# Kernel tuning notes

Measured on AMD Instinct MI355X. Metric: run time of the kernel, lower is better.

## Reference

```python
import jax, jax.numpy as jnp
import numpy as np

ACT_BITS = 8
Q_B = 2 ** (ACT_BITS - 1)          # 128
EPS = 1e-6                          # module epsilon
GN_EPS = 1e-5                       # torch GroupNorm default eps
SCALE = 0.01                        # fixed ternary weight scale (buffer)
STRIDE = 1
PADDING = 1


def setup_inputs() -> dict:
    key = jax.random.key(0)
    k1, k2 = jax.random.split(key)
    x = jax.random.normal(k1, (16, 256, 64, 64), dtype=jnp.float32)
    weight = jax.random.normal(k2, (256, 256, 3, 3), dtype=jnp.float32)
    bias = jnp.zeros((256,), dtype=jnp.float32)
    ln_weight = jnp.ones((256,), dtype=jnp.float32)
    ln_bias = jnp.zeros((256,), dtype=jnp.float32)
    return {"x": x, "weight": weight, "bias": bias,
            "ln_weight": ln_weight, "ln_bias": ln_bias}


def _group_norm_1group(x, gamma, beta):
    # GroupNorm(1, C): normalize over (C, H, W) per sample, per-channel affine.
    mean = jnp.mean(x, axis=(1, 2, 3), keepdims=True)
    var = jnp.var(x, axis=(1, 2, 3), keepdims=True)
    xn = (x - mean) * jax.lax.rsqrt(var + GN_EPS)
    return xn * gamma[None, :, None, None] + beta[None, :, None, None]


def reference(x, weight, bias, ln_weight, ln_bias):
    # 1) GroupNorm
    x_ln = _group_norm_1group(x, ln_weight, ln_bias)

    # 2) BitNet absmax activation quantization (global absmax)
    gamma = jnp.maximum(jnp.max(jnp.abs(x_ln)), EPS)
    x_scaled = x_ln * (Q_B / gamma)
    x_clipped = jnp.clip(x_scaled, -Q_B + EPS, Q_B - EPS)
    x_quant = jnp.round(x_clipped)

    # 3) Ternary weight quantization with fixed scale: {-SCALE, 0, +SCALE}
    delta = 0.7 * jnp.mean(jnp.abs(weight))  # TTQ threshold
    w_q = jnp.where(weight > delta, SCALE,
                    jnp.where(weight < -delta, -SCALE, 0.0)).astype(weight.dtype)

    # 4) Conv2d (NCHW, OIHW)
    y = jax.lax.conv_general_dilated(
        x_quant, w_q,
        window_strides=(STRIDE, STRIDE),
        padding=[(PADDING, PADDING), (PADDING, PADDING)],
        dimension_numbers=("NCHW", "OIHW", "NCHW"),
        feature_group_count=1,
    )

    # 5) Dequant + bias
    y = y * (gamma / Q_B) + bias[None, :, None, None]
    return y
```

## Files before the change

kernel.cpp:

```cpp
#include <hip/hip_runtime.h>
#include <hip/hip_bf16.h>

#define CHW   1048576
#define XQ_BYTES 17842176u
#define WQ_OFF   17842176u
#define GNP_OFF  18432000u
#define CMM_OFF  18448384u
#define MR_OFF   18481152u
#define SC_OFF   18481280u
#define WP_OFF   18481296u
#define DL_OFF   18481584u
#define EVC_OFF  18481588u
#define EVL_OFF  18481592u

typedef __attribute__((ext_vector_type(4)))  int i32x4;
typedef __attribute__((ext_vector_type(16))) int i32x16;

__device__ __forceinline__ void gload16(const void* g, void* l) {
    __builtin_amdgcn_global_load_lds(
        (const __attribute__((address_space(1))) unsigned int*)(unsigned long long)(g),
        (__attribute__((address_space(3))) unsigned int*)(unsigned int)(unsigned long long)(l),
        16, 0, 0);
}

__global__ void k_pass1(const float* __restrict__ x, double2* __restrict__ part,
                        float2* __restrict__ cmm) {
    int bid = blockIdx.x;
    int n = bid >> 6, c4 = bid & 63;
    int t = threadIdx.x, ch = t >> 6, lane = t & 63;
    int c = c4 * 4 + ch;
    const float4* p = (const float4*)(x + (size_t)n * CHW + (size_t)c * 4096);
    double s = 0.0, ss = 0.0;
    float mn = 1e30f, mx = -1e30f;
#pragma unroll
    for (int k = 0; k < 16; ++k) {
        float4 v = p[k * 64 + lane];
        mn = fminf(mn, fminf(fminf(v.x, v.y), fminf(v.z, v.w)));
        mx = fmaxf(mx, fmaxf(fmaxf(v.x, v.y), fmaxf(v.z, v.w)));
        double dx = v.x, dy = v.y, dz = v.z, dw = v.w;
        s  += dx + dy + dz + dw;
        ss += dx * dx + dy * dy + dz * dz + dw * dw;
    }
    for (int o = 32; o; o >>= 1) {
        s += __shfl_down(s, o); ss += __shfl_down(ss, o);
        mn = fminf(mn, __shfl_down(mn, o)); mx = fmaxf(mx, __shfl_down(mx, o));
    }
    __shared__ double sh0[4], sh1[4];
    if (lane == 0) {
        cmm[n * 256 + c] = make_float2(mn, mx);
        sh0[ch] = s; sh1[ch] = ss;
    }
    __syncthreads();
    if (t == 0)
        part[bid] = make_double2(sh0[0] + sh0[1] + sh0[2] + sh0[3],
                                 sh1[0] + sh1[1] + sh1[2] + sh1[3]);
}

__global__ void k_wsum(const float* __restrict__ w, double* __restrict__ wp) {
    int blk = blockIdx.x, t = threadIdx.x;
    const float4* p = (const float4*)(w + (size_t)blk * 16384);
    double s = 0.0;
#pragma unroll
    for (int j = 0; j < 16; ++j) {
        float4 v = p[j * 256 + t];
        s += fabs((double)v.x) + fabs((double)v.y) + fabs((double)v.z) + fabs((double)v.w);
    }
    for (int o = 32; o; o >>= 1) s += __shfl_down(s, o);
    __shared__ double sh[4];
    if ((t & 63) == 0) sh[t >> 6] = s;
    __syncthreads();
    if (t == 0) wp[blk] = sh[0] + sh[1] + sh[2] + sh[3];
}

__global__ void k_scalars(const double2* __restrict__ part, const float2* __restrict__ cmm,
                          const float* __restrict__ lnw, const float* __restrict__ lnb,
                          const double* __restrict__ wp,
                          float2* __restrict__ mr, float* __restrict__ sc,
                          float* __restrict__ dl, int* __restrict__ evcnt) {
    __shared__ float shm[16], shr[16];
    int t = threadIdx.x;
    {
        int n = t >> 4, i = t & 15;
        double s = 0.0, ss = 0.0;
#pragma unroll
        for (int k = 0; k < 4; ++k) {
            double2 v = part[n * 64 + i * 4 + k];
            s += v.x; ss += v.y;
        }
        for (int o = 8; o; o >>= 1) { s += __shfl_down(s, o); ss += __shfl_down(ss, o); }
        if (i == 0) {
            double mean = s * (1.0 / 1048576.0);
            double var  = ss * (1.0 / 1048576.0) - mean * mean;
            shm[n] = (float)mean; shr[n] = (float)(1.0 / sqrt(var + 1e-5));
        }
    }
    __syncthreads();
    if (t < 16) mr[t] = make_float2(shm[t], shr[t]);
    if (t == 0) evcnt[0] = 0;
    float m = 0.0f;
#pragma unroll
    for (int k = 0; k < 16; ++k) {
        int idx = t + k * 256;
        int n = idx >> 8, c = idx & 255;
        float2 v = cmm[idx];
        float scale = lnw[c] * shr[n];
        float shift = lnb[c] - shm[n] * scale;
        m = fmaxf(m, fmaxf(fabsf(v.x * scale + shift), fabsf(v.y * scale + shift)));
    }
    for (int o = 32; o; o >>= 1) m = fmaxf(m, __shfl_down(m, o));
    __shared__ float shg[4];
    if ((t & 63) == 0) shg[t >> 6] = m;
    __syncthreads();
    if (t == 0) {
        float gamma = fmaxf(fmaxf(fmaxf(shg[0], shg[1]), fmaxf(shg[2], shg[3])), 1e-6f);
        sc[0] = gamma;
        sc[1] = 128.0f / gamma;
        sc[2] = (gamma / 128.0f) * 0.01f;
    }
    if (t < 64) {
        double s = (t < 36) ? wp[t] : 0.0;
        for (int o = 32; o; o >>= 1) s += __shfl_down(s, o);
        if (t == 0) dl[0] = (float)(0.7 * (s / 589824.0));
    }
}

__global__ void k_wquant(const float* __restrict__ w, const float* __restrict__ dl,
                         signed char* __restrict__ wq) {
    __shared__ float sw[2304];
    int co = blockIdx.x, t = threadIdx.x;
    const float* wr = w + (size_t)co * 2304;
#pragma unroll
    for (int j = 0; j < 9; ++j) sw[j * 256 + t] = wr[j * 256 + t];
    __syncthreads();
    float d = dl[0];
#pragma unroll
    for (int tap = 0; tap < 9; ++tap) {
        float v = sw[t * 9 + tap];
        int s = (v > d) ? 1 : ((v < -d) ? -1 : 0);
        wq[tap * 65536 + co * 256 + t] = (signed char)s;
    }
}

__global__ void k_halo(unsigned char* __restrict__ xq) {
    int idx = blockIdx.x * 8 + (threadIdx.x >> 5);
    int n = idx / 260, p = idx - n * 260;
    int hh, ww;
    if (p < 66)       { hh = 0;        ww = p; }
    else if (p < 132) { hh = 65;       ww = p - 66; }
    else if (p < 196) { hh = p - 131;  ww = 0; }
    else              { hh = p - 195;  ww = 65; }
    *(uint2*)(xq + ((size_t)(n * 66 + hh) * 66 + ww) * 256 + (threadIdx.x & 31) * 8) =
        make_uint2(0, 0);
}

__global__ void k_quantx(const float* __restrict__ x, const float2* __restrict__ mr,
                         const float* __restrict__ sc, const float* __restrict__ lnw,
                         const float* __restrict__ lnb, unsigned char* __restrict__ xq,
                         int* __restrict__ evcnt, int* __restrict__ evlist) {
    int bid = blockIdx.x;
    int n = bid >> 6, hg = (bid >> 2) & 15, cg = bid & 3;
    int t = threadIdx.x;
    int w = t & 63, h = hg * 4 + (t >> 6);
    float2 m = mr[n];
    float s128 = sc[1];
    uint u[16];
    const float* xp = x + (((size_t)n * 256 + cg * 64) * 64 + h) * 64 + w;
#pragma unroll
    for (int ci = 0; ci < 64; ++ci) {
        int c = cg * 64 + ci;
        float g = lnw[c] * m.y;
        float be = lnb[c];
        float v = xp[(size_t)ci * 4096];
        float xs = ((v - m.x) * g + be) * s128;
        xs = fminf(fmaxf(xs, -(128.0f - 1e-6f)), 128.0f - 1e-6f);
        int q = (int)rintf(xs);
        if (q == 128) {
            int idx = atomicAdd(evcnt, 1);
            if (idx < 1024) evlist[idx] = (n << 20) | (h << 14) | (w << 8) | c;
            q = 127;
        }
        uint b = (uint)(q & 255);
        if ((ci & 3) == 0) u[ci >> 2] = b; else u[ci >> 2] |= b << ((ci & 3) * 8);
    }
    unsigned char* op = xq + ((size_t)(n * 66 + h + 1) * 66 + (w + 1)) * 256 + cg * 64;
    uint4* o4 = (uint4*)op;
#pragma unroll
    for (int s2 = 0; s2 < 4; ++s2)
        o4[s2] = make_uint4(u[s2 * 4], u[s2 * 4 + 1], u[s2 * 4 + 2], u[s2 * 4 + 3]);
}

__global__ void k_fix(const signed char* __restrict__ wq, const int* __restrict__ evcnt,
                      const int* __restrict__ evlist, const float* __restrict__ sc,
                      float* __restrict__ out) {
    int cnt = *evcnt; if (cnt > 1024) cnt = 1024;
    float qs = sc[2];
    int co = threadIdx.x;
    for (int e = blockIdx.x; e < cnt; e += gridDim.x) {
        int pk = evlist[e];
        int n = pk >> 20, h = (pk >> 14) & 63, w = (pk >> 8) & 63, ci = pk & 255;
#pragma unroll
        for (int ty = 0; ty < 3; ++ty)
#pragma unroll
            for (int tx = 0; tx < 3; ++tx) {
                int i = h + 1 - ty, j = w + 1 - tx;
                if (i < 0 || i > 63 || j < 0 || j > 63) continue;
                int sgn = wq[(ty * 3 + tx) * 65536 + co * 256 + ci];
                if (sgn)
                    atomicAdd(out + (((size_t)n * 256 + co) * 64 + i) * 64 + j,
                              qs * (float)sgn);
            }
    }
}

#define ABUFB 32768
#define LD16(off) (*(const i32x4*)&lds8[(off)])
#define MFMA_I8(A, B, C) __builtin_amdgcn_mfma_i32_32x32x32_i8(A, B, C, 0, 0, 0)

#define STAGE_A(AS) { \
    const int _so = (AS) * ABUFB + wv * 1024; \
    gload16(aSrc + stA,         lds8 + _so); \
    gload16(aSrc + stA + 33792, lds8 + _so + 8192); \
    if (aKc < 3) { aKc++; stA += 64; } \
    else { aKc = 0; if (aTx < 2) { aTx++; stA += 64; } else { aTx = 0; stA += 16192; } } }

#define STAGE_B(BS) { \
    const int _so = (BS) * ABUFB + 16384 + wv * 1024; \
    gload16(bSrc + stB,         lds8 + _so); \
    gload16(bSrc + stB + 32768, lds8 + _so + 8192); \
    if (bKc < 3) { bKc++; stB += 64; } else { bKc = 0; stB += 65344; } }

#define STEP(R) { \
    const int _ab = (R) * ABUFB; \
    const int _bb = (R) * ABUFB + 16384; \
    i32x4 b00 = LD16(_bb + rdB);          i32x4 b01 = LD16((_bb + rdB) ^ 32); \
    i32x4 b10 = LD16(_bb + rdB + 2048);   i32x4 b11 = LD16((_bb + rdB + 2048) ^ 32); \
    _Pragma("unroll") \
    for (int _m = 0; _m < 4; ++_m) { \
        const int _ra = _ab + rdA + _m * 2048; \
        i32x4 a0 = LD16(_ra); \
        i32x4 a1 = LD16(_ra ^ 32); \
        __builtin_amdgcn_s_setprio(1); \
        acc[_m][0] = MFMA_I8(a0, b00, acc[_m][0]); \
        acc[_m][1] = MFMA_I8(a0, b10, acc[_m][1]); \
        acc[_m][0] = MFMA_I8(a1, b01, acc[_m][0]); \
        acc[_m][1] = MFMA_I8(a1, b11, acc[_m][1]); \
        __builtin_amdgcn_s_setprio(0); \
    } }

#define PITER(R0, R1, S0, S1, DO0, DO1, W) { \
    if (DO0) { STAGE_A(S0) STAGE_B(S0) } \
    if (DO1) { STAGE_A(S1) STAGE_B(S1) } \
    STEP(R0) \
    STEP(R1) \
    if ((W) == 4)      { asm volatile("s_waitcnt vmcnt(4)" ::: "memory"); } \
    else if ((W) == 0) { asm volatile("s_waitcnt vmcnt(0)" ::: "memory"); } \
    if ((W) >= 0) { __builtin_amdgcn_s_barrier(); __builtin_amdgcn_sched_barrier(0); } \
}

#define STORE4(P, A, BV) { \
    float4 v0; v0.x = (float)(A)[0]*qs+(BV);  v0.y = (float)(A)[1]*qs+(BV);  v0.z = (float)(A)[2]*qs+(BV);  v0.w = (float)(A)[3]*qs+(BV);  *(float4*)((P))      = v0; \
    float4 v1; v1.x = (float)(A)[4]*qs+(BV);  v1.y = (float)(A)[5]*qs+(BV);  v1.z = (float)(A)[6]*qs+(BV);  v1.w = (float)(A)[7]*qs+(BV);  *(float4*)((P) + 8)  = v1; \
    float4 v2; v2.x = (float)(A)[8]*qs+(BV);  v2.y = (float)(A)[9]*qs+(BV);  v2.z = (float)(A)[10]*qs+(BV); v2.w = (float)(A)[11]*qs+(BV); *(float4*)((P) + 16) = v2; \
    float4 v3; v3.x = (float)(A)[12]*qs+(BV); v3.y = (float)(A)[13]*qs+(BV); v3.z = (float)(A)[14]*qs+(BV); v3.w = (float)(A)[15]*qs+(BV); *(float4*)((P) + 24) = v3; }

__global__ __launch_bounds__(512, 2) void k_conv(const unsigned char* __restrict__ xq,
                                                 const signed char* __restrict__ wq,
                                                 const float* __restrict__ sc,
                                                 const float* __restrict__ bias,
                                                 float* __restrict__ out) {
    __shared__ __align__(128) unsigned char lds8[163840];
    int t = threadIdx.x, wv = t >> 6, l = t & 63;
    int wm = wv >> 2, wn = wv & 3;
    int l31 = l & 31, l5 = l >> 5;

    int bid = ((int)blockIdx.x & 7) * 32 + ((int)blockIdx.x >> 3);
    int n = bid >> 4, h2 = (bid & 15) << 2;

    int s_src = (l & 7) ^ (l >> 3);
    int sb2   = (s_src >> 2) & 1;
    int skc   = s_src & 3;
    int RA    = wv * 16 + ((l >> 3) << 1) + sb2;
    int hsub  = RA >> 6, wA = RA & 63;
    const unsigned char* aSrc = xq +
        ((size_t)(n * 66 + h2 + hsub) * 66 + wA) * 256 + skc * 16;
    int coB = ((wv * 8 + (l >> 3)) << 1) + sb2;
    const unsigned char* bSrc = (const unsigned char*)wq + (size_t)coB * 256 + skc * 16;

    int q3    = (l31 >> 1) & 7;
    int s0    = ((l31 & 1) << 2) | l5;
    int phys0 = s0 ^ q3;
    int rdA = (wm * 64 + (l31 >> 1)) * 128 + phys0 * 16;
    int rdB = (wn * 32 + (l31 >> 1)) * 128 + phys0 * 16;

    i32x16 acc[4][2] = {};

    int stA = 0, aKc = 0, aTx = 0;
    int stB = 0, bKc = 0;
    STAGE_A(0) STAGE_B(0)
    STAGE_A(1) STAGE_B(1)
    STAGE_A(2) STAGE_B(2)
    asm volatile("s_waitcnt vmcnt(4)" ::: "memory");
    __builtin_amdgcn_s_barrier();
    __builtin_amdgcn_sched_barrier(0);

#pragma unroll 1
    for (int it = 0; it < 3; ++it) {
        PITER(0, 1, 3, 4, 1, 1, 4)
        PITER(2, 3, 0, 1, 1, 1, 4)
        PITER(4, 0, 2, 3, 1, 1, 4)
        PITER(1, 2, 4, 0, 1, 1, 4)
        PITER(3, 4, 1, 2, 1, 1, 4)
    }
    PITER(0, 1, 3, 4, 1, 1, 4)
    PITER(2, 3, 0, 0, 1, 0, 0)
    PITER(4, 0, 0, 0, 0, 0, -1)

    float qs = sc[2];
#pragma unroll
    for (int m = 0; m < 4; ++m) {
        int h = h2 + wm * 2 + (m >> 1);
        int wb = (m & 1) * 32 + l5 * 4;
        size_t obase = (size_t)n * CHW + (size_t)h * 64 + wb;
#pragma unroll
        for (int nf = 0; nf < 2; ++nf) {
            int co = wn * 64 + nf * 32 + l31;
            float bv = bias[co];
            float* ob = out + obase + (size_t)co * 4096;
            STORE4(ob, acc[m][nf], bv)
        }
    }
}

extern "C" void kernel_launch(void* const* d_in, const int* in_sizes, int n_in,
                              void* d_out, int out_size, void* d_ws, size_t ws_size,
                              hipStream_t stream) {
    (void)in_sizes; (void)n_in; (void)out_size; (void)ws_size;
    const float* x    = (const float*)d_in[0];
    const float* wgt  = (const float*)d_in[1];
    const float* bias = (const float*)d_in[2];
    const float* lnw  = (const float*)d_in[3];
    const float* lnb  = (const float*)d_in[4];
    float* out = (float*)d_out;
    char* ws = (char*)d_ws;

    unsigned char* xq  = (unsigned char*)ws;
    signed char*   wq  = (signed char*)(ws + WQ_OFF);
    double2* gnp = (double2*)(ws + GNP_OFF);
    float2*  cmm = (float2*)(ws + CMM_OFF);
    float2*  mr  = (float2*)(ws + MR_OFF);
    float*   sc  = (float*)(ws + SC_OFF);
    double*  wp  = (double*)(ws + WP_OFF);
    float*   dl  = (float*)(ws + DL_OFF);
    int*     evc = (int*)(ws + EVC_OFF);
    int*     evl = (int*)(ws + EVL_OFF);

    k_pass1  <<<1024, 256, 0, stream>>>(x, gnp, cmm);
    k_wsum   <<<36,   256, 0, stream>>>(wgt, wp);
    k_scalars<<<1,    256, 0, stream>>>(gnp, cmm, lnw, lnb, wp, mr, sc, dl, evc);
    k_wquant <<<256,  256, 0, stream>>>(wgt, dl, wq);
    k_halo   <<<520,  256, 0, stream>>>(xq);
    k_quantx <<<1024, 256, 0, stream>>>(x, mr, sc, lnw, lnb, xq, evc, evl);
    k_conv   <<<256,  512, 0, stream>>>(xq, wq, sc, bias, out);
    k_fix    <<<64,   256, 0, stream>>>(wq, evc, evl, sc, out);
}
```

Baseline: 105.1 us.

## Restructure int8 conv main loop into single-buffer phases and stage epilogue through LDS

Each pipeline iteration now handles one LDS buffer. All A and B fragments are loaded into registers first, then the next global→LDS stage is issued, then a barrier is taken before the 16 MFMAs run. The deeper vmcnt(8) wait keeps more async loads in flight. The epilogue now writes dequantized results into a swizzled LDS tile and then issues coalesced float4 stores to the NCHW output, replacing the strided per-lane stores. In exchange, each phase adds barriers and the output path adds two LDS round trips with syncthreads.

```diff
diff --git a/kernel.cpp b/kernel.cpp
--- a/kernel.cpp
+++ b/kernel.cpp
@@ -229,39 +229,35 @@
     gload16(bSrc + stB + 32768, lds8 + _so + 8192); \
     if (bKc < 3) { bKc++; stB += 64; } else { bKc = 0; stB += 65344; } }
 
-#define STEP(R) { \
-    const int _ab = (R) * ABUFB; \
-    const int _bb = (R) * ABUFB + 16384; \
-    i32x4 b00 = LD16(_bb + rdB);          i32x4 b01 = LD16((_bb + rdB) ^ 32); \
-    i32x4 b10 = LD16(_bb + rdB + 2048);   i32x4 b11 = LD16((_bb + rdB + 2048) ^ 32); \
-    _Pragma("unroll") \
-    for (int _m = 0; _m < 4; ++_m) { \
-        const int _ra = _ab + rdA + _m * 2048; \
-        i32x4 a0 = LD16(_ra); \
-        i32x4 a1 = LD16(_ra ^ 32); \
-        __builtin_amdgcn_s_setprio(1); \
-        acc[_m][0] = MFMA_I8(a0, b00, acc[_m][0]); \
-        acc[_m][1] = MFMA_I8(a0, b10, acc[_m][1]); \
-        acc[_m][0] = MFMA_I8(a1, b01, acc[_m][0]); \
-        acc[_m][1] = MFMA_I8(a1, b11, acc[_m][1]); \
-        __builtin_amdgcn_s_setprio(0); \
-    } }
-
-#define PITER(R0, R1, S0, S1, DO0, DO1, W) { \
-    if (DO0) { STAGE_A(S0) STAGE_B(S0) } \
-    if (DO1) { STAGE_A(S1) STAGE_B(S1) } \
-    STEP(R0) \
-    STEP(R1) \
-    if ((W) == 4)      { asm volatile("s_waitcnt vmcnt(4)" ::: "memory"); } \
+#define PHASE(RB, SB, DO, W) { \
+    const int _ab = (RB) * ABUFB; \
+    const int _bb = (RB) * ABUFB + 16384; \
+    i32x4 a00 = LD16(_ab + rdA),        a01 = LD16((_ab + rdA) ^ 32); \
+    i32x4 a10 = LD16(_ab + rdA + 2048), a11 = LD16((_ab + rdA + 2048) ^ 32); \
+    i32x4 a20 = LD16(_ab + rdA + 4096), a21 = LD16((_ab + rdA + 4096) ^ 32); \
+    i32x4 a30 = LD16(_ab + rdA + 6144), a31 = LD16((_ab + rdA + 6144) ^ 32); \
+    i32x4 b00 = LD16(_bb + rdB),        b01 = LD16((_bb + rdB) ^ 32); \
+    i32x4 b10 = LD16(_bb + rdB + 2048), b11 = LD16((_bb + rdB + 2048) ^ 32); \
+    if (DO) { STAGE_A(SB) STAGE_B(SB) } \
+    __builtin_amdgcn_sched_barrier(0); \
+    __builtin_amdgcn_s_barrier(); \
+    asm volatile("s_waitcnt lgkmcnt(0)" ::: "memory"); \
+    __builtin_amdgcn_sched_barrier(0); \
+    __builtin_amdgcn_s_setprio(1); \
+    acc[0][0] = MFMA_I8(a00, b00, acc[0][0]); acc[0][1] = MFMA_I8(a00, b10, acc[0][1]); \
+    acc[1][0] = MFMA_I8(a10, b00, acc[1][0]); acc[1][1] = MFMA_I8(a10, b10, acc[1][1]); \
+    acc[2][0] = MFMA_I8(a20, b00, acc[2][0]); acc[2][1] = MFMA_I8(a20, b10, acc[2][1]); \
+    acc[3][0] = MFMA_I8(a30, b00, acc[3][0]); acc[3][1] = MFMA_I8(a30, b10, acc[3][1]); \
+    acc[0][0] = MFMA_I8(a01, b01, acc[0][0]); acc[0][1] = MFMA_I8(a01, b11, acc[0][1]); \
+    acc[1][0] = MFMA_I8(a11, b01, acc[1][0]); acc[1][1] = MFMA_I8(a11, b11, acc[1][1]); \
+    acc[2][0] = MFMA_I8(a21, b01, acc[2][0]); acc[2][1] = MFMA_I8(a21, b11, acc[2][1]); \
+    acc[3][0] = MFMA_I8(a31, b01, acc[3][0]); acc[3][1] = MFMA_I8(a31, b11, acc[3][1]); \
+    __builtin_amdgcn_s_setprio(0); \
+    if ((W) == 8)      { asm volatile("s_waitcnt vmcnt(8)" ::: "memory"); } \
+    else if ((W) == 4) { asm volatile("s_waitcnt vmcnt(4)" ::: "memory"); } \
     else if ((W) == 0) { asm volatile("s_waitcnt vmcnt(0)" ::: "memory"); } \
     if ((W) >= 0) { __builtin_amdgcn_s_barrier(); __builtin_amdgcn_sched_barrier(0); } \
 }
-
-#define STORE4(P, A, BV) { \
-    float4 v0; v0.x = (float)(A)[0]*qs+(BV);  v0.y = (float)(A)[1]*qs+(BV);  v0.z = (float)(A)[2]*qs+(BV);  v0.w = (float)(A)[3]*qs+(BV);  *(float4*)((P))      = v0; \
-    float4 v1; v1.x = (float)(A)[4]*qs+(BV);  v1.y = (float)(A)[5]*qs+(BV);  v1.z = (float)(A)[6]*qs+(BV);  v1.w = (float)(A)[7]*qs+(BV);  *(float4*)((P) + 8)  = v1; \
-    float4 v2; v2.x = (float)(A)[8]*qs+(BV);  v2.y = (float)(A)[9]*qs+(BV);  v2.z = (float)(A)[10]*qs+(BV); v2.w = (float)(A)[11]*qs+(BV); *(float4*)((P) + 16) = v2; \
-    float4 v3; v3.x = (float)(A)[12]*qs+(BV); v3.y = (float)(A)[13]*qs+(BV); v3.z = (float)(A)[14]*qs+(BV); v3.w = (float)(A)[15]*qs+(BV); *(float4*)((P) + 24) = v3; }
 
 __global__ __launch_bounds__(512, 2) void k_conv(const unsigned char* __restrict__ xq,
                                                  const signed char* __restrict__ wq,
@@ -299,35 +295,62 @@
     STAGE_A(0) STAGE_B(0)
     STAGE_A(1) STAGE_B(1)
     STAGE_A(2) STAGE_B(2)
-    asm volatile("s_waitcnt vmcnt(4)" ::: "memory");
+    asm volatile("s_waitcnt vmcnt(8)" ::: "memory");
     __builtin_amdgcn_s_barrier();
     __builtin_amdgcn_sched_barrier(0);
 
 #pragma unroll 1
-    for (int it = 0; it < 3; ++it) {
-        PITER(0, 1, 3, 4, 1, 1, 4)
-        PITER(2, 3, 0, 1, 1, 1, 4)
-        PITER(4, 0, 2, 3, 1, 1, 4)
-        PITER(1, 2, 4, 0, 1, 1, 4)
-        PITER(3, 4, 1, 2, 1, 1, 4)
-    }
-    PITER(0, 1, 3, 4, 1, 1, 4)
-    PITER(2, 3, 0, 0, 1, 0, 0)
-    PITER(4, 0, 0, 0, 0, 0, -1)
+    for (int it = 0; it < 6; ++it) {
+        PHASE(0, 3, 1, 8)
+        PHASE(1, 4, 1, 8)
+        PHASE(2, 0, 1, 8)
+        PHASE(3, 1, 1, 8)
+        PHASE(4, 2, 1, 8)
+    }
+    PHASE(0, 3, 1, 8)
+    PHASE(1, 4, 1, 8)
+    PHASE(2, 0, 1, 8)
+    PHASE(3, 0, 0, 4)
+    PHASE(4, 0, 0, 0)
+    PHASE(0, 0, 0, -1)
 
     float qs = sc[2];
-#pragma unroll
-    for (int m = 0; m < 4; ++m) {
-        int h = h2 + wm * 2 + (m >> 1);
-        int wb = (m & 1) * 32 + l5 * 4;
-        size_t obase = (size_t)n * CHW + (size_t)h * 64 + wb;
-#pragma unroll
-        for (int nf = 0; nf < 2; ++nf) {
-            int co = wn * 64 + nf * 32 + l31;
-            float bv = bias[co];
-            float* ob = out + obase + (size_t)co * 4096;
-            STORE4(ob, acc[m][nf], bv)
-        }
+    float bv0 = bias[wn * 64 + l31];
+    float bv1 = bias[wn * 64 + 32 + l31];
+    __builtin_amdgcn_s_barrier();
+    float4* lf = (float4*)lds8;
+#pragma unroll
+    for (int rh = 0; rh < 2; ++rh) {
+#pragma unroll
+        for (int mh = 0; mh < 2; ++mh) {
+            int m = rh * 2 + mh;
+#pragma unroll
+            for (int nf = 0; nf < 2; ++nf) {
+                int co = wn * 64 + nf * 32 + l31;
+                float bv = nf ? bv1 : bv0;
+                int rowb = (wm * 256 + co) * 16;
+#pragma unroll
+                for (int rg = 0; rg < 4; ++rg) {
+                    int slot = mh * 8 + rg * 2 + l5;
+                    float4 v;
+                    v.x = (float)acc[m][nf][rg * 4 + 0] * qs + bv;
+                    v.y = (float)acc[m][nf][rg * 4 + 1] * qs + bv;
+                    v.z = (float)acc[m][nf][rg * 4 + 2] * qs + bv;
+                    v.w = (float)acc[m][nf][rg * 4 + 3] * qs + bv;
+                    lf[rowb + (slot ^ (co & 7))] = v;
+                }
+            }
+        }
+        __syncthreads();
+#pragma unroll
+        for (int i = 0; i < 16; ++i) {
+            int idx = t + i * 512;
+            int lw = idx & 15, co = (idx >> 4) & 255, hs = idx >> 12;
+            float4 v = lf[(hs * 256 + co) * 16 + (lw ^ (co & 7))];
+            int h = h2 + hs * 2 + rh;
+            *(float4*)(out + ((size_t)(n * 256 + co) * 64 + h) * 64 + lw * 4) = v;
+        }
+        if (rh == 0) __syncthreads();
     }
 }
 
```

After: 102.2 us. 2.7% less time.
